# Optimization experiments

Hardware: AMD Instinct MI355X
Metric: run time of the kernel (lower is better)

## Reference

```python
import jax, jax.numpy as jnp
import numpy as np

N_NODES = 100000


def _gcn_norm(edge_index, num_nodes):
    # PyG GCNConv default: add self-loops, symmetric normalization
    src, dst = edge_index[0], edge_index[1]
    loop = jnp.arange(num_nodes, dtype=src.dtype)
    src = jnp.concatenate([src, loop])
    dst = jnp.concatenate([dst, loop])
    deg = jax.ops.segment_sum(jnp.ones_like(dst, dtype=jnp.float32), dst,
                              num_segments=num_nodes)
    dinv = jnp.where(deg > 0, jax.lax.rsqrt(deg), 0.0)
    norm = dinv[src] * dinv[dst]  # [E + N]
    return src, dst, norm


def _gcn_conv(x, W, b, src, dst, norm, num_nodes):
    h = x @ W                                   # [N, out] linear first (PyG)
    msg = h[src] * norm[:, None]                # gather + scale  [E+N, out]
    out = jax.ops.segment_sum(msg, dst, num_segments=num_nodes)  # scatter-add
    return out + b


def setup_inputs() -> dict:
    key = jax.random.key(0)
    ks = jax.random.split(key, 5)
    x = jax.random.normal(ks[0], (N_NODES, 3), dtype=jnp.float32)
    edge_index = jax.random.randint(ks[1], (2, 1600000), 0, N_NODES, dtype=jnp.int64)
    # Glorot-ish weights, zero bias (PyG defaults)
    W1 = jax.random.normal(ks[2], (3, 64), dtype=jnp.float32) * (1.0 / np.sqrt(3))
    W2 = jax.random.normal(ks[3], (64, 64), dtype=jnp.float32) * (1.0 / np.sqrt(64))
    W3 = jax.random.normal(ks[4], (64, 3), dtype=jnp.float32) * (1.0 / np.sqrt(64))
    b1 = jnp.zeros((64,), jnp.float32)
    b2 = jnp.zeros((64,), jnp.float32)
    b3 = jnp.zeros((3,), jnp.float32)
    return {"x": x, "edge_index": edge_index, "W1": W1, "b1": b1,
            "W2": W2, "b2": b2, "W3": W3, "b3": b3}


def reference(x, edge_index, W1, b1, W2, b2, W3, b3):
    n = x.shape[0]
    src, dst, norm = _gcn_norm(edge_index, n)  # same graph for every layer
    h = jax.nn.relu(_gcn_conv(x, W1, b1, src, dst, norm, n))
    h = jax.nn.relu(_gcn_conv(h, W2, b2, src, dst, norm, n))
    return _gcn_conv(h, W3, b3, src, dst, norm, n)
```

## Files before the change

kernel.cpp:

```cpp
#include <hip/hip_runtime.h>

#define TPB 256
#define NB 391
#define CH 4096
#define BS 4736


__device__ __forceinline__ unsigned bpack(float a, float b) {
    unsigned ua = __float_as_uint(a), ub = __float_as_uint(b);
    ua = (ua + 0x7fffu + ((ua >> 16) & 1u)) >> 16;
    ub = (ub + 0x7fffu + ((ub >> 16) & 1u)) >> 16;
    return ua | (ub << 16);
}
__device__ __forceinline__ float blo(unsigned u) { return __uint_as_float(u << 16); }
__device__ __forceinline__ float bhi(unsigned u) { return __uint_as_float(u & 0xffff0000u); }


__global__ __launch_bounds__(TPB) void k_placeA(const int* __restrict__ src,
                                                const int* __restrict__ dst,
                                                unsigned* __restrict__ gcur,
                                                unsigned* __restrict__ bkt, int E) {
    __shared__ unsigned val[CH];
    __shared__ unsigned dstS[CH];
    __shared__ unsigned short bid[CH];
    __shared__ unsigned cnt[512], loff[512], lcur[512], basev[512];
    __shared__ unsigned tsum[TPB];
    int t = threadIdx.x;
    int c0 = blockIdx.x * CH;
    int n = E - c0; if (n > CH) n = CH;

    for (int b = t; b < 512; b += TPB) { cnt[b] = 0; lcur[b] = 0; }
    __syncthreads();
    for (int i = t; i < n; i += TPB) {
        unsigned d = (unsigned)dst[c0 + i];
        dstS[i] = d;
        atomicAdd(&cnt[d >> 8], 1u);
    }
    __syncthreads();
    for (int b = t; b < NB; b += TPB)
        basev[b] = cnt[b] ? atomicAdd(&gcur[b], cnt[b]) : 0u;
    unsigned a0 = cnt[2 * t], a1 = cnt[2 * t + 1];
    tsum[t] = a0 + a1;
    __syncthreads();
#pragma unroll
    for (int o = 1; o < TPB; o <<= 1) {
        unsigned v = (t >= o) ? tsum[t - o] : 0u;
        __syncthreads();
        tsum[t] += v;
        __syncthreads();
    }
    unsigned ex = tsum[t] - (a0 + a1);
    loff[2 * t] = ex; loff[2 * t + 1] = ex + a0;
    __syncthreads();
    for (int i = t; i < n; i += TPB) {
        unsigned s = (unsigned)src[c0 + i];
        unsigned d = dstS[i];
        unsigned b = d >> 8;
        unsigned r = atomicAdd(&lcur[b], 1u);
        unsigned slot = loff[b] + r;
        val[slot] = s | ((d & 255u) << 20);
        bid[slot] = (unsigned short)b;
    }
    __syncthreads();
    for (int i = t; i < n; i += TPB) {
        unsigned b = bid[i];
        bkt[(size_t)b * BS + basev[b] + ((unsigned)i - loff[b])] = val[i];
    }
}


__global__ __launch_bounds__(512) void k_fineS(const unsigned* __restrict__ bkt,
                                               const unsigned* __restrict__ gcur,
                                               const float* __restrict__ x,
                                               int2* __restrict__ rp2,
                                               int* __restrict__ ssrc,
                                               float* __restrict__ dinv,
                                               float4* __restrict__ xs4,
                                               unsigned* __restrict__ gdh, int N) {
    __shared__ unsigned bins[4096];
    __shared__ unsigned tsum[512];
    __shared__ unsigned degS[256];
    __shared__ unsigned dh[64];
    __shared__ unsigned bs[BS];
    int t = threadIdx.x, b = blockIdx.x;
    for (int i = t; i < 4096; i += 512) bins[i] = 0;
    if (t < 64) dh[t] = 0;
    __syncthreads();
    int p0 = b * BS;
    int n = (int)gcur[b];
    for (int i = t; i < n; i += 512) {
        unsigned u = bkt[p0 + i];
        bs[i] = u;
        unsigned bin = ((u >> 20) << 4) | ((u & 0xFFFFFu) >> 13);
        atomicAdd(&bins[bin], 1u);
    }
    __syncthreads();
    unsigned s[8], pre[8];
#pragma unroll
    for (int i = 0; i < 8; ++i) s[i] = bins[8 * t + i];
    if (t < 256) {
        unsigned d = 0;
#pragma unroll
        for (int i = 0; i < 16; ++i) d += bins[(t << 4) + i];
        degS[t] = d;
    }
    unsigned tot = 0;
#pragma unroll
    for (int i = 0; i < 8; ++i) { pre[i] = tot; tot += s[i]; }
    tsum[t] = tot;
    __syncthreads();
#pragma unroll
    for (int o = 1; o < 512; o <<= 1) {
        unsigned v = (t >= o) ? tsum[t - o] : 0u;
        __syncthreads();
        tsum[t] += v;
        __syncthreads();
    }
    unsigned ex = tsum[t] - tot;
#pragma unroll
    for (int i = 0; i < 8; ++i) bins[8 * t + i] = ex + pre[i];
    __syncthreads();
    if (t < 256) {
        int node = (b << 8) + t;
        if (node < N) {
            unsigned c = degS[t];
            atomicAdd(&dh[c < 63u ? c : 63u], 1u);
            int beg = p0 + (int)bins[t << 4];
            rp2[node] = make_int2(beg, beg + (int)c);
            float dv = rsqrtf((float)(c + 1u));
            dinv[node] = dv;
            float4 xv;
            xv.x = x[node * 3 + 0] * dv;
            xv.y = x[node * 3 + 1] * dv;
            xv.z = x[node * 3 + 2] * dv;
            xv.w = 0.f;
            xs4[node] = xv;
        }
    }
    __syncthreads();
    if (t < 64 && dh[t]) atomicAdd(&gdh[t], dh[t]);
    for (int i = t; i < n; i += 512) {
        unsigned u = bs[i];
        unsigned bin = ((u >> 20) << 4) | ((u & 0xFFFFFu) >> 13);
        unsigned r = atomicAdd(&bins[bin], 1u);
        ssrc[p0 + (int)r] = (int)(u & 0xFFFFFu);
    }
}


__global__ __launch_bounds__(64) void k_dscan(const unsigned* __restrict__ gdh,
                                              unsigned* __restrict__ dcur) {
    int t = threadIdx.x;
    unsigned v = gdh[t];
    unsigned sum = v;
#pragma unroll
    for (int o = 1; o < 64; o <<= 1) {
        unsigned u = __shfl_up(sum, o, 64);
        if (t >= o) sum += u;
    }
    unsigned total = __shfl(sum, 63, 64);
    dcur[t] = total - sum;
}


__global__ __launch_bounds__(TPB) void k_dperm(const int2* __restrict__ rp2,
                                               unsigned* __restrict__ dcur,
                                               int* __restrict__ perm, int N) {
    __shared__ unsigned dh[64], basev[64], lcur[64];
    int t = threadIdx.x;
    int node = blockIdx.x * TPB + t;
    if (t < 64) { dh[t] = 0; lcur[t] = 0; }
    __syncthreads();
    int bin = -1;
    if (node < N) {
        int2 r = rp2[node];
        unsigned d = (unsigned)(r.y - r.x);
        bin = d < 63u ? (int)d : 63;
        atomicAdd(&dh[bin], 1u);
    }
    __syncthreads();
    if (t < 64) basev[t] = dh[t] ? atomicAdd(&dcur[t], dh[t]) : 0u;
    __syncthreads();
    if (node < N) {
        unsigned rk = atomicAdd(&lcur[bin], 1u);
        perm[basev[bin] + rk] = node;
    }
}


__global__ __launch_bounds__(TPB) void k_l1q(const float* __restrict__ xs4,
                                             const int2* __restrict__ rp2,
                                             const int* __restrict__ ssrc,
                                             const float* __restrict__ dinv,
                                             const int* __restrict__ perm,
                                             const float* __restrict__ W1,
                                             const float* __restrict__ b1,
                                             const float* __restrict__ W2,
                                             uint4* __restrict__ gb, int N) {
    __shared__ unsigned Ws2[2048];
    for (int i = threadIdx.x; i < 2048; i += TPB)
        Ws2[i] = bpack(W2[2 * i], W2[2 * i + 1]);
    __syncthreads();
    int tid = blockIdx.x * TPB + threadIdx.x;
    int slot = tid >> 2, c = tid & 3;
    if (slot >= N) return;
    int node = perm[slot];
    int2 r = rp2[node];
    float acc = xs4[(node << 2) + c];
    int j = r.x;
    for (; j + 3 < r.y; j += 4) {
        int s0 = ssrc[j], s1 = ssrc[j+1], s2 = ssrc[j+2], s3 = ssrc[j+3];
        acc += (xs4[(s0 << 2) + c] + xs4[(s1 << 2) + c])
             + (xs4[(s2 << 2) + c] + xs4[(s3 << 2) + c]);
    }
    for (; j < r.y; ++j) acc += xs4[(ssrc[j] << 2) + c];
    float dv = dinv[node];
    acc *= dv;
    int base = (threadIdx.x & 63) & ~3;
    float q0 = __shfl(acc, base + 0, 64);
    float q1 = __shfl(acc, base + 1, 64);
    float q2 = __shfl(acc, base + 2, 64);

    float o[16];
#pragma unroll
    for (int i = 0; i < 16; ++i) o[i] = 0.f;
    const int cofs8 = c << 3;
    for (int kb = 0; kb < 16; ++kb) {
        int k0 = __builtin_amdgcn_readfirstlane(kb) << 2;
        const float* W1k = W1 + k0;
        const float* b1k = b1 + k0;
        float h[4];
        h[0] = fmaxf(fmaf(q0, W1k[0], fmaf(q1, W1k[64], fmaf(q2, W1k[128], b1k[0]))), 0.f);
        h[1] = fmaxf(fmaf(q0, W1k[1], fmaf(q1, W1k[65], fmaf(q2, W1k[129], b1k[1]))), 0.f);
        h[2] = fmaxf(fmaf(q0, W1k[2], fmaf(q1, W1k[66], fmaf(q2, W1k[130], b1k[2]))), 0.f);
        h[3] = fmaxf(fmaf(q0, W1k[3], fmaf(q1, W1k[67], fmaf(q2, W1k[131], b1k[3]))), 0.f);
#pragma unroll
        for (int kk = 0; kk < 4; ++kk) {
            const uint4* Wp = (const uint4*)(Ws2 + ((k0 + kk) << 5) + cofs8);
            uint4 wA = Wp[0];
            uint4 wB = Wp[1];
            float hv = h[kk];
            o[0]  = fmaf(hv, blo(wA.x), o[0]);  o[1]  = fmaf(hv, bhi(wA.x), o[1]);
            o[2]  = fmaf(hv, blo(wA.y), o[2]);  o[3]  = fmaf(hv, bhi(wA.y), o[3]);
            o[4]  = fmaf(hv, blo(wA.z), o[4]);  o[5]  = fmaf(hv, bhi(wA.z), o[5]);
            o[6]  = fmaf(hv, blo(wA.w), o[6]);  o[7]  = fmaf(hv, bhi(wA.w), o[7]);
            o[8]  = fmaf(hv, blo(wB.x), o[8]);  o[9]  = fmaf(hv, bhi(wB.x), o[9]);
            o[10] = fmaf(hv, blo(wB.y), o[10]); o[11] = fmaf(hv, bhi(wB.y), o[11]);
            o[12] = fmaf(hv, blo(wB.z), o[12]); o[13] = fmaf(hv, bhi(wB.z), o[13]);
            o[14] = fmaf(hv, blo(wB.w), o[14]); o[15] = fmaf(hv, bhi(wB.w), o[15]);
        }
    }
    uint4 v0, v1;
    v0.x = bpack(o[0] * dv,  o[1] * dv);
    v0.y = bpack(o[2] * dv,  o[3] * dv);
    v0.z = bpack(o[4] * dv,  o[5] * dv);
    v0.w = bpack(o[6] * dv,  o[7] * dv);
    v1.x = bpack(o[8] * dv,  o[9] * dv);
    v1.y = bpack(o[10] * dv, o[11] * dv);
    v1.z = bpack(o[12] * dv, o[13] * dv);
    v1.w = bpack(o[14] * dv, o[15] * dv);
    uint4* gp = gb + ((size_t)node << 3) + (c << 1);
    gp[0] = v0;
    gp[1] = v1;
}


__global__ __launch_bounds__(TPB) void k_p2fb(const uint4* __restrict__ gb,
                                              const int2* __restrict__ rp2,
                                              const int* __restrict__ ssrc,
                                              const float* __restrict__ dinv,
                                              const int* __restrict__ perm,
                                              const float* __restrict__ b2,
                                              const float* __restrict__ W3,
                                              float* __restrict__ q4, int N) {
    int tid = blockIdx.x * TPB + threadIdx.x;
    int slot = tid >> 3, q = tid & 7;
    if (slot >= N) return;
    int node = perm[slot];
    int2 r = rp2[node];
    int beg = r.x, end = r.y;
    float a[8];
    {
        uint4 u = gb[((size_t)node << 3) + q];
        a[0] = blo(u.x); a[1] = bhi(u.x);
        a[2] = blo(u.y); a[3] = bhi(u.y);
        a[4] = blo(u.z); a[5] = bhi(u.z);
        a[6] = blo(u.w); a[7] = bhi(u.w);
    }
    int j = beg;
    for (; j + 3 < end; j += 4) {
        int s0 = ssrc[j], s1 = ssrc[j+1], s2 = ssrc[j+2], s3 = ssrc[j+3];
        uint4 u0 = gb[((size_t)s0 << 3) + q];
        uint4 u1 = gb[((size_t)s1 << 3) + q];
        uint4 u2 = gb[((size_t)s2 << 3) + q];
        uint4 u3 = gb[((size_t)s3 << 3) + q];
        a[0] += (blo(u0.x) + blo(u1.x)) + (blo(u2.x) + blo(u3.x));
        a[1] += (bhi(u0.x) + bhi(u1.x)) + (bhi(u2.x) + bhi(u3.x));
        a[2] += (blo(u0.y) + blo(u1.y)) + (blo(u2.y) + blo(u3.y));
        a[3] += (bhi(u0.y) + bhi(u1.y)) + (bhi(u2.y) + bhi(u3.y));
        a[4] += (blo(u0.z) + blo(u1.z)) + (blo(u2.z) + blo(u3.z));
        a[5] += (bhi(u0.z) + bhi(u1.z)) + (bhi(u2.z) + bhi(u3.z));
        a[6] += (blo(u0.w) + blo(u1.w)) + (blo(u2.w) + blo(u3.w));
        a[7] += (bhi(u0.w) + bhi(u1.w)) + (bhi(u2.w) + bhi(u3.w));
    }
    for (; j < end; ++j) {
        uint4 u = gb[((size_t)ssrc[j] << 3) + q];
        a[0] += blo(u.x); a[1] += bhi(u.x);
        a[2] += blo(u.y); a[3] += bhi(u.y);
        a[4] += blo(u.z); a[5] += bhi(u.z);
        a[6] += blo(u.w); a[7] += bhi(u.w);
    }
    float dv = dinv[node];
    int f0 = q << 3;
    const float* bb = b2 + f0;
    const float* Wr = W3 + f0 * 3;
    float p0 = 0.f, p1 = 0.f, p2 = 0.f;
#pragma unroll
    for (int i = 0; i < 8; ++i) {
        float h = fmaxf(fmaf(a[i], dv, bb[i]), 0.f);
        p0 = fmaf(h, Wr[3*i+0], p0);
        p1 = fmaf(h, Wr[3*i+1], p1);
        p2 = fmaf(h, Wr[3*i+2], p2);
    }
#pragma unroll
    for (int off = 1; off < 8; off <<= 1) {
        p0 += __shfl_xor(p0, off, 64);
        p1 += __shfl_xor(p1, off, 64);
        p2 += __shfl_xor(p2, off, 64);
    }
    if (q < 4) {
        float v = (q == 0) ? p0 * dv : (q == 1) ? p1 * dv : (q == 2) ? p2 * dv : 0.f;
        q4[((size_t)node << 2) + q] = v;
    }
}


__global__ __launch_bounds__(TPB) void k_pull3o(const float* __restrict__ g34,
                                                const int2* __restrict__ rp2,
                                                const int* __restrict__ ssrc,
                                                const float* __restrict__ dinv,
                                                const float* __restrict__ b3,
                                                float* __restrict__ out, int N) {
    int tid = blockIdx.x * TPB + threadIdx.x;
    int node = tid >> 2, c = tid & 3;
    if (node >= N) return;
    int2 r = rp2[node];
    int beg = r.x, end = r.y;
    float acc = g34[tid];
    int j = beg;
    for (; j + 3 < end; j += 4) {
        int s0 = ssrc[j], s1 = ssrc[j+1], s2 = ssrc[j+2], s3 = ssrc[j+3];
        acc += (g34[(s0 << 2) + c] + g34[(s1 << 2) + c])
             + (g34[(s2 << 2) + c] + g34[(s3 << 2) + c]);
    }
    for (; j < end; ++j) acc += g34[(ssrc[j] << 2) + c];
    if (c < 3) out[(size_t)node * 3 + c] = dinv[node] * acc + b3[c];
}

extern "C" void kernel_launch(void* const* d_in, const int* in_sizes, int n_in,
                              void* d_out, int out_size, void* d_ws, size_t ws_size,
                              hipStream_t stream) {
    const float* x  = (const float*)d_in[0];
    const int*   ei = (const int*)  d_in[1];
    const float* W1 = (const float*)d_in[2];
    const float* b1 = (const float*)d_in[3];
    const float* W2 = (const float*)d_in[4];
    const float* b2 = (const float*)d_in[5];
    const float* W3 = (const float*)d_in[6];
    const float* b3 = (const float*)d_in[7];
    float* out = (float*)d_out;

    const int N = in_sizes[0] / 3;
    const int E = in_sizes[1] / 2;
    const int* srcI = ei;
    const int* dstI = ei + E;

    float*    ws   = (float*)d_ws;
    unsigned* gcur = (unsigned*)ws;
    unsigned* gdh  = (unsigned*)(ws + 512);
    unsigned* dcur = (unsigned*)(ws + 576);
    int*      perm = (int*)     (ws + 640);
    int2*     rp2  = (int2*)    (ws + 640 + N);
    float*    dinv = ws + 640 + 3 * (size_t)N;
    int*      ssrc = (int*)     (dinv + N);
    float*    xs4  = (float*)(ssrc + (size_t)NB * BS);
    float*    q4   = xs4 + (size_t)N * 4;
    unsigned* gb   = (unsigned*)(q4 + (size_t)N * 4);
    unsigned* bkt  = gb + (size_t)N * 32;

    int gPlace = (E + CH - 1) / CH;
    int gS3    = (N * 4 + TPB - 1) / TPB;
    int gP2    = (int)(((size_t)N * 8 + TPB - 1) / TPB);
    int gN     = (N + TPB - 1) / TPB;

    hipMemsetAsync(gcur, 0, 576 * sizeof(unsigned), stream);
    k_placeA<<<gPlace, TPB, 0, stream>>>(srcI, dstI, gcur, bkt, E);
    k_fineS <<<NB,     512, 0, stream>>>(bkt, gcur, x, rp2, ssrc, dinv,
                                         (float4*)xs4, gdh, N);
    k_dscan <<<1,       64, 0, stream>>>(gdh, dcur);
    k_dperm <<<gN,     TPB, 0, stream>>>(rp2, dcur, perm, N);

    k_l1q<<<gS3, TPB, 0, stream>>>(xs4, rp2, ssrc, dinv, perm,
                                   W1, b1, W2, (uint4*)gb, N);

    k_p2fb<<<gP2, TPB, 0, stream>>>((const uint4*)gb, rp2, ssrc, dinv, perm,
                                    b2, W3, q4, N);

    k_pull3o<<<gS3, TPB, 0, stream>>>(q4, rp2, ssrc, dinv, b3, out, N);
}
```

Baseline: 204.0 us.

## Split layer-1 gather from dense transform into separate kernels

The fused layer-1 kernel is split in two. The first kernel does the 3-channel neighbor gather in natural node order and writes the scaled aggregate plus dinv to a new float4 buffer. The second kernel computes relu(qW1+b1)·W2 with one thread per node-half, reading W2 as fp32 from global with wave-uniform addresses instead of bf16-packed LDS, and writes 32 outputs per thread. This removes the per-block LDS staging and the 3-of-4-thread redundant dense work, at the cost of an extra launch, a round trip through global memory and more registers per thread.

```diff
diff --git a/kernel.cpp b/kernel.cpp
--- a/kernel.cpp
+++ b/kernel.cpp
@@ -188,25 +188,16 @@
 }
 
 
-__global__ __launch_bounds__(TPB) void k_l1q(const float* __restrict__ xs4,
-                                             const int2* __restrict__ rp2,
-                                             const int* __restrict__ ssrc,
-                                             const float* __restrict__ dinv,
-                                             const int* __restrict__ perm,
-                                             const float* __restrict__ W1,
-                                             const float* __restrict__ b1,
-                                             const float* __restrict__ W2,
-                                             uint4* __restrict__ gb, int N) {
-    __shared__ unsigned Ws2[2048];
-    for (int i = threadIdx.x; i < 2048; i += TPB)
-        Ws2[i] = bpack(W2[2 * i], W2[2 * i + 1]);
-    __syncthreads();
+__global__ __launch_bounds__(TPB) void k_gq(const float* __restrict__ xs4,
+                                            const int2* __restrict__ rp2,
+                                            const int* __restrict__ ssrc,
+                                            const float* __restrict__ dinv,
+                                            float* __restrict__ qx4, int N) {
     int tid = blockIdx.x * TPB + threadIdx.x;
-    int slot = tid >> 2, c = tid & 3;
-    if (slot >= N) return;
-    int node = perm[slot];
+    int node = tid >> 2, c = tid & 3;
+    if (node >= N) return;
     int2 r = rp2[node];
-    float acc = xs4[(node << 2) + c];
+    float acc = xs4[tid];
     int j = r.x;
     for (; j + 3 < r.y; j += 4) {
         int s0 = ssrc[j], s1 = ssrc[j+1], s2 = ssrc[j+2], s3 = ssrc[j+3];
@@ -215,16 +206,25 @@
     }
     for (; j < r.y; ++j) acc += xs4[(ssrc[j] << 2) + c];
     float dv = dinv[node];
-    acc *= dv;
-    int base = (threadIdx.x & 63) & ~3;
-    float q0 = __shfl(acc, base + 0, 64);
-    float q1 = __shfl(acc, base + 1, 64);
-    float q2 = __shfl(acc, base + 2, 64);
-
-    float o[16];
-#pragma unroll
-    for (int i = 0; i < 16; ++i) o[i] = 0.f;
-    const int cofs8 = c << 3;
+    qx4[tid] = (c < 3) ? acc * dv : dv;
+}
+
+
+__global__ __launch_bounds__(TPB) void k_l1d(const float4* __restrict__ qx4,
+                                             const float* __restrict__ W1,
+                                             const float* __restrict__ b1,
+                                             const float* __restrict__ W2,
+                                             uint4* __restrict__ gb, int N) {
+    int t = threadIdx.x;
+    int node = blockIdx.x * 128 + (t & 127);
+    int half = __builtin_amdgcn_readfirstlane(t >> 7);
+    if (node >= N) return;
+    float4 qv = qx4[node];
+    float q0 = qv.x, q1 = qv.y, q2 = qv.z, dv = qv.w;
+    float o[32];
+#pragma unroll
+    for (int i = 0; i < 32; ++i) o[i] = 0.f;
+    const int fofs = half << 5;
     for (int kb = 0; kb < 16; ++kb) {
         int k0 = __builtin_amdgcn_readfirstlane(kb) << 2;
         const float* W1k = W1 + k0;
@@ -236,32 +236,23 @@
         h[3] = fmaxf(fmaf(q0, W1k[3], fmaf(q1, W1k[67], fmaf(q2, W1k[131], b1k[3]))), 0.f);
 #pragma unroll
         for (int kk = 0; kk < 4; ++kk) {
-            const uint4* Wp = (const uint4*)(Ws2 + ((k0 + kk) << 5) + cofs8);
-            uint4 wA = Wp[0];
-            uint4 wB = Wp[1];
+            const float* Wr = W2 + ((k0 + kk) << 6) + fofs;
             float hv = h[kk];
-            o[0]  = fmaf(hv, blo(wA.x), o[0]);  o[1]  = fmaf(hv, bhi(wA.x), o[1]);
-            o[2]  = fmaf(hv, blo(wA.y), o[2]);  o[3]  = fmaf(hv, bhi(wA.y), o[3]);
-            o[4]  = fmaf(hv, blo(wA.z), o[4]);  o[5]  = fmaf(hv, bhi(wA.z), o[5]);
-            o[6]  = fmaf(hv, blo(wA.w), o[6]);  o[7]  = fmaf(hv, bhi(wA.w), o[7]);
-            o[8]  = fmaf(hv, blo(wB.x), o[8]);  o[9]  = fmaf(hv, bhi(wB.x), o[9]);
-            o[10] = fmaf(hv, blo(wB.y), o[10]); o[11] = fmaf(hv, bhi(wB.y), o[11]);
-            o[12] = fmaf(hv, blo(wB.z), o[12]); o[13] = fmaf(hv, bhi(wB.z), o[13]);
-            o[14] = fmaf(hv, blo(wB.w), o[14]); o[15] = fmaf(hv, bhi(wB.w), o[15]);
+#pragma unroll
+            for (int i = 0; i < 32; ++i)
+                o[i] = fmaf(hv, Wr[i], o[i]);
         }
     }
-    uint4 v0, v1;
-    v0.x = bpack(o[0] * dv,  o[1] * dv);
-    v0.y = bpack(o[2] * dv,  o[3] * dv);
-    v0.z = bpack(o[4] * dv,  o[5] * dv);
-    v0.w = bpack(o[6] * dv,  o[7] * dv);
-    v1.x = bpack(o[8] * dv,  o[9] * dv);
-    v1.y = bpack(o[10] * dv, o[11] * dv);
-    v1.z = bpack(o[12] * dv, o[13] * dv);
-    v1.w = bpack(o[14] * dv, o[15] * dv);
-    uint4* gp = gb + ((size_t)node << 3) + (c << 1);
-    gp[0] = v0;
-    gp[1] = v1;
+    uint4* gp = gb + ((size_t)node << 3) + (half << 2);
+#pragma unroll
+    for (int g8 = 0; g8 < 4; ++g8) {
+        uint4 v;
+        v.x = bpack(o[8*g8+0] * dv, o[8*g8+1] * dv);
+        v.y = bpack(o[8*g8+2] * dv, o[8*g8+3] * dv);
+        v.z = bpack(o[8*g8+4] * dv, o[8*g8+5] * dv);
+        v.w = bpack(o[8*g8+6] * dv, o[8*g8+7] * dv);
+        gp[g8] = v;
+    }
 }
 
 
@@ -385,13 +376,15 @@
     int*      ssrc = (int*)     (dinv + N);
     float*    xs4  = (float*)(ssrc + (size_t)NB * BS);
     float*    q4   = xs4 + (size_t)N * 4;
-    unsigned* gb   = (unsigned*)(q4 + (size_t)N * 4);
+    float*    qx4  = q4  + (size_t)N * 4;
+    unsigned* gb   = (unsigned*)(qx4 + (size_t)N * 4);
     unsigned* bkt  = gb + (size_t)N * 32;
 
     int gPlace = (E + CH - 1) / CH;
     int gS3    = (N * 4 + TPB - 1) / TPB;
     int gP2    = (int)(((size_t)N * 8 + TPB - 1) / TPB);
     int gN     = (N + TPB - 1) / TPB;
+    int gL1    = (N + 127) / 128;
 
     hipMemsetAsync(gcur, 0, 576 * sizeof(unsigned), stream);
     k_placeA<<<gPlace, TPB, 0, stream>>>(srcI, dstI, gcur, bkt, E);
@@ -400,8 +393,9 @@
     k_dscan <<<1,       64, 0, stream>>>(gdh, dcur);
     k_dperm <<<gN,     TPB, 0, stream>>>(rp2, dcur, perm, N);
 
-    k_l1q<<<gS3, TPB, 0, stream>>>(xs4, rp2, ssrc, dinv, perm,
-                                   W1, b1, W2, (uint4*)gb, N);
+    k_gq <<<gS3, TPB, 0, stream>>>(xs4, rp2, ssrc, dinv, qx4, N);
+    k_l1d<<<gL1, TPB, 0, stream>>>((const float4*)qx4, W1, b1, W2,
+                                   (uint4*)gb, N);
 
     k_p2fb<<<gP2, TPB, 0, stream>>>((const uint4*)gb, rp2, ssrc, dinv, perm,
                                     b2, W3, q4, N);
```

Result: no change. 200.9 us (-1.5%).
